# Kernel optimization log

Measured on AMD Instinct MI355X. Metric: run time of the kernel, lower is better.

## Reference

```python
import jax, jax.numpy as jnp
import numpy as np

N_NODES = 50000
N_EDGES = 600000
F_NODE = 128
F_EDGE = 32
MSG = 32


def setup_inputs() -> dict:
    key = jax.random.key(0)
    k1, k2, k3, k4, k5, k6, k7 = jax.random.split(key, 7)
    node_features = jax.random.normal(k1, (N_NODES, F_NODE), dtype=jnp.float32)
    edge_node_indices = jax.random.randint(k2, (2, N_EDGES), 0, N_NODES, dtype=jnp.int64)
    edge_features = jax.random.normal(k3, (N_EDGES, F_EDGE), dtype=jnp.float32)
    edge_in = 2 * F_NODE + F_EDGE  # 288
    node_in = F_NODE + MSG  # 160
    s_e = 1.0 / np.sqrt(edge_in)
    s_n = 1.0 / np.sqrt(node_in)
    We = jax.random.uniform(k4, (edge_in, MSG), dtype=jnp.float32, minval=-s_e, maxval=s_e)
    be = jax.random.uniform(k5, (MSG,), dtype=jnp.float32, minval=-s_e, maxval=s_e)
    Wn = jax.random.uniform(k6, (node_in, F_NODE), dtype=jnp.float32, minval=-s_n, maxval=s_n)
    bn = jax.random.uniform(k7, (F_NODE,), dtype=jnp.float32, minval=-s_n, maxval=s_n)
    return {
        "node_features": node_features,
        "edge_node_indices": edge_node_indices,
        "edge_features": edge_features,
        "We": We, "be": be, "Wn": Wn, "bn": bn,
    }


def reference(node_features, edge_node_indices, edge_features, We, be, Wn, bn):
    node0, node1 = edge_node_indices[0], edge_node_indices[1]
    # gather endpoint features per edge: [E, 2*Fn + Fe]
    msg_in = jnp.concatenate(
        [node_features[node0], node_features[node1], edge_features], axis=1
    )
    messages = jax.nn.relu(msg_in @ We + be)  # [E, MSG]
    # scatter-sum messages into source nodes (scatter index = node0)
    msg_sums = jax.ops.segment_sum(messages, node0, num_segments=node_features.shape[0])
    node_in = jnp.concatenate([node_features, msg_sums], axis=1)  # [N, Fn+MSG]
    return jax.nn.relu(node_in @ Wn + bn)  # [N, Fn]
```

## Files before the change

kernel.cpp:

```cpp
#include <hip/hip_runtime.h>

#define N_NODES 50000
#define N_EDGES 600000
#define F_NODE 128
#define F_EDGE 32
#define MSG 32
#define NPB 32
#define CHK 128
#define QB64 ((N_NODES + 63) / 64)
#define FBLOCKS ((N_NODES + NPB - 1) / NPB)
#define CBLOCKS ((N_EDGES + 255) / 256)

__device__ __forceinline__ unsigned short f2bf(float f) {
    union { float f; unsigned int u; } v; v.f = f;
    unsigned int r = v.u + 0x7fffu + ((v.u >> 16) & 1u);
    return (unsigned short)(r >> 16);
}

#define BAR_LGKM() do {                                           \
    asm volatile("s_waitcnt lgkmcnt(0)" ::: "memory");            \
    __builtin_amdgcn_s_barrier();                                 \
    asm volatile("" ::: "memory");                                \
} while (0)

__global__ __launch_bounds__(256)
void qcount_kernel(const float* __restrict__ nf,
                   const float* __restrict__ We,
                   const float* __restrict__ be,
                   const int* __restrict__ idx,
                   unsigned short* __restrict__ Q,
                   unsigned short* __restrict__ P0g,
                   int* __restrict__ deg)
{
    if (blockIdx.x >= QB64) {
        int e = (blockIdx.x - QB64) * 256 + threadIdx.x;
        if (e < N_EDGES) {
            int n = idx[e];
            if ((unsigned)n < (unsigned)N_NODES) atomicAdd(&deg[n], 1);
        }
        return;
    }
    __shared__ float sInT[32 * 64];
    __shared__ float sWeA[32 * 32];
    __shared__ float sWeB[32 * 32];

    const int tid = threadIdx.x;
    const int n0b = blockIdx.x * 64;
    const int ng = tid & 31;
    const int og = tid >> 5;

    float accA[2][4], accB[2][4];
#pragma unroll
    for (int i = 0; i < 2; ++i)
#pragma unroll
        for (int j = 0; j < 4; ++j) { accA[i][j] = 0.f; accB[i][j] = 0.f; }

    for (int kc = 0; kc < 4; ++kc) {
        __syncthreads();
        ((float4*)sWeA)[tid] = ((const float4*)(We + kc * 32 * MSG))[tid];
        ((float4*)sWeB)[tid] = ((const float4*)(We + (128 + kc * 32) * MSG))[tid];
        {
            int nl = tid >> 2, q = tid & 3;
            int n = n0b + nl; if (n >= N_NODES) n = N_NODES - 1;
            const float4* src4 = (const float4*)(nf + (size_t)n * F_NODE + kc * 32);
#pragma unroll
            for (int h = 0; h < 2; ++h) {
                float4 v = src4[q * 2 + h];
                int kl = q * 8 + h * 4;
                sInT[(kl + 0) * 64 + nl] = v.x;
                sInT[(kl + 1) * 64 + nl] = v.y;
                sInT[(kl + 2) * 64 + nl] = v.z;
                sInT[(kl + 3) * 64 + nl] = v.w;
            }
        }
        __syncthreads();
#pragma unroll
        for (int k = 0; k < 32; ++k) {
            float2 m = *(const float2*)&sInT[k * 64 + 2 * ng];
            float4 wa = *(const float4*)&sWeA[k * 32 + og * 4];
            float4 wb = *(const float4*)&sWeB[k * 32 + og * 4];
            accA[0][0] += m.x * wa.x; accA[0][1] += m.x * wa.y;
            accA[0][2] += m.x * wa.z; accA[0][3] += m.x * wa.w;
            accA[1][0] += m.y * wa.x; accA[1][1] += m.y * wa.y;
            accA[1][2] += m.y * wa.z; accA[1][3] += m.y * wa.w;
            accB[0][0] += m.x * wb.x; accB[0][1] += m.x * wb.y;
            accB[0][2] += m.x * wb.z; accB[0][3] += m.x * wb.w;
            accB[1][0] += m.y * wb.x; accB[1][1] += m.y * wb.y;
            accB[1][2] += m.y * wb.z; accB[1][3] += m.y * wb.w;
        }
    }
    float bloc[4];
#pragma unroll
    for (int j = 0; j < 4; ++j) bloc[j] = be[og * 4 + j];
#pragma unroll
    for (int i = 0; i < 2; ++i) {
        int n = n0b + 2 * ng + i;
        if (n < N_NODES) {
            ushort4 oq, op;
            oq.x = f2bf(accB[i][0]); oq.y = f2bf(accB[i][1]);
            oq.z = f2bf(accB[i][2]); oq.w = f2bf(accB[i][3]);
            op.x = f2bf(accA[i][0] + bloc[0]); op.y = f2bf(accA[i][1] + bloc[1]);
            op.z = f2bf(accA[i][2] + bloc[2]); op.w = f2bf(accA[i][3] + bloc[3]);
            *(ushort4*)(Q   + (size_t)n * MSG + og * 4) = oq;
            *(ushort4*)(P0g + (size_t)n * MSG + og * 4) = op;
        }
    }
}

__global__ __launch_bounds__(1024)
void scan_kernel(int* __restrict__ deg_cursor) {
    __shared__ int wsum[16];
    __shared__ int wpre[16];
    const int t = threadIdx.x;
    const int lane = t & 63;
    const int wid = t >> 6;
    const int N4 = N_NODES / 4;
    const int NT = (N4 + 1023) / 1024;
    int run = 0;
    int4 vnext = make_int4(0, 0, 0, 0);
    if (t < N4) vnext = ((const int4*)deg_cursor)[t];
    for (int tt = 0; tt < NT; ++tt) {
        int4 v = vnext;
        if (tt + 1 < NT) {
            int ni = (tt + 1) * 1024 + t;
            vnext = (ni < N4) ? ((const int4*)deg_cursor)[ni] : make_int4(0, 0, 0, 0);
        }
        int s = v.x + v.y + v.z + v.w;
        int x = s;
#pragma unroll
        for (int d = 1; d < 64; d <<= 1) {
            int u = __shfl_up(x, (unsigned)d, 64);
            if (lane >= d) x += u;
        }
        if (lane == 63) wsum[wid] = x;
        BAR_LGKM();
        if (wid == 0) {
            int ss = (lane < 16) ? wsum[lane] : 0;
#pragma unroll
            for (int d = 1; d < 16; d <<= 1) {
                int u = __shfl_up(ss, (unsigned)d, 64);
                if (lane >= d) ss += u;
            }
            if (lane < 16) wpre[lane] = ss;
        }
        BAR_LGKM();
        int wexcl = (wid > 0) ? wpre[wid - 1] : 0;
        int total = wpre[15];
        int i4 = tt * 1024 + t;
        if (i4 < N4) {
            int base = run + wexcl + (x - s);
            int4 o;
            o.x = base;
            o.y = base + v.x;
            o.z = base + v.x + v.y;
            o.w = base + v.x + v.y + v.z;
            ((int4*)deg_cursor)[i4] = o;
        }
        run += total;
        BAR_LGKM();
    }
}

__global__ void scatter_kernel(const int* __restrict__ idx, int* __restrict__ cursor,
                               int* __restrict__ perm) {
    int e = blockIdx.x * 256 + threadIdx.x;
    if (e < N_EDGES) {
        int n = idx[e];
        if ((unsigned)n >= (unsigned)N_NODES) n = 0;
        int p = atomicAdd(&cursor[n], 1);
        if ((unsigned)p < (unsigned)N_EDGES) perm[p] = e;
    }
}

__global__ __launch_bounds__(256, 5)
void fused_kernel(const float* __restrict__ nf,
                  const int* __restrict__ idx,
                  const float* __restrict__ ef,
                  const float* __restrict__ We,
                  const float* __restrict__ Wn,
                  const float* __restrict__ bn,
                  const int* __restrict__ perm,
                  const int* __restrict__ cursor,
                  const unsigned short* __restrict__ Q,
                  const unsigned short* __restrict__ P0g,
                  float* __restrict__ out)
{
    __shared__ __align__(16) float S[5284];
    float* sBuf = S;
    float* sWeC = S + 4096;
    float* sInT2 = S + 4096;
    int* sOff = (int*)(S + 5120);
    int* sNL  = (int*)(S + 5153);

    const int tid = threadIdx.x;
    const int n0b = blockIdx.x * NPB;

    if (tid <= NPB) {
        int nn = n0b + tid - 1;
        int v;
        if (nn < 0) v = 0;
        else { if (nn >= N_NODES) nn = N_NODES - 1; v = cursor[nn]; }
        if (v < 0) v = 0;
        if (v > N_EDGES) v = N_EDGES;
        sOff[tid] = v;
    }
    ((float4*)sWeC)[tid] = ((const float4*)(We + 256 * MSG))[tid];
    __syncthreads();

    const int rs = sOff[0];
    const int re = sOff[NPB];

    float msum[4];
#pragma unroll
    for (int j = 0; j < 4; ++j) msum[j] = 0.f;
    const int rnl = tid >> 3;
    const int rq4 = (tid & 7) * 4;
    const int gx  = (rq4 >> 3) << 2;

    const int eg = tid & 63;
    const int og = tid >> 6;
    const int el = tid >> 1;
    const int h2 = tid & 1;

    int n1r = 0;
    int pe_next = 0, pe_next2 = 0;
    float4 efr[4];
#pragma unroll
    for (int q = 0; q < 4; ++q) efr[q] = make_float4(0.f, 0.f, 0.f, 0.f);

    if (rs < re) {
        int e0 = rs + el;
        int pe0 = 0;
        if (e0 < re) {
            pe0 = perm[e0];
            if ((unsigned)pe0 >= (unsigned)N_EDGES) pe0 = 0;
            if (h2 == 0) {
                int tn = idx[N_EDGES + pe0];
                if ((unsigned)tn >= (unsigned)N_NODES) tn = 0;
                n1r = tn;
            }
        }
        const float4* ef4 = (const float4*)(ef + (size_t)pe0 * F_EDGE + h2 * 16);
#pragma unroll
        for (int q = 0; q < 4; ++q) efr[q] = ef4[q];
        int e1 = rs + CHK + el;
        if (e1 < re) {
            int p = perm[e1];
            if ((unsigned)p >= (unsigned)N_EDGES) p = 0;
            pe_next = p;
        }
        pe_next2 = pe_next;
    }

    for (int cs = rs; cs < re; cs += CHK) {
        BAR_LGKM();
        pe_next = pe_next2;
        {
#pragma unroll
            for (int q = 0; q < 4; ++q) {
                float4 v = efr[q];
                int g = (h2 * 2 + (q >> 1)) & 3;
                int ctw = ((el & ~3) ^ (g << 2)) + (el & 3);
                int r0 = (h2 * 16 + q * 4) * CHK;
                sBuf[r0 + 0 * CHK + ctw] = v.x;
                sBuf[r0 + 1 * CHK + ctw] = v.y;
                sBuf[r0 + 2 * CHK + ctw] = v.z;
                sBuf[r0 + 3 * CHK + ctw] = v.w;
            }
            if (h2 == 0) {
                int e = cs + el;
                int ln = 0;
                if (e < re) {
                    int lo = 0, hi = NPB;
#pragma unroll
                    for (int s = 0; s < 5; ++s) {
                        int mid = (lo + hi) >> 1;
                        if (sOff[mid] <= e) lo = mid; else hi = mid;
                    }
                    ln = lo;
                }
                sNL[el] = (ln << 20) | n1r;
            }
            int e1 = cs + CHK + el;
            if (e1 < re) {
                int pe1 = pe_next;
                if (h2 == 0) {
                    int tn = idx[N_EDGES + pe1];
                    if ((unsigned)tn >= (unsigned)N_NODES) tn = 0;
                    n1r = tn;
                }
                const float4* ef4 = (const float4*)(ef + (size_t)pe1 * F_EDGE + h2 * 16);
#pragma unroll
                for (int q = 0; q < 4; ++q) efr[q] = ef4[q];
            } else if (h2 == 0) n1r = 0;
            int e2 = cs + 2 * CHK + el;
            if (e2 < re) {
                int p = perm[e2];
                if ((unsigned)p >= (unsigned)N_EDGES) p = 0;
                pe_next2 = p;
            } else pe_next2 = 0;
        }
        BAR_LGKM();

        int nlv0 = sNL[2 * eg], nlv1 = sNL[2 * eg + 1];
        uint4 qv[2], pv[2];
        qv[0] = *(const uint4*)(Q   + (size_t)(nlv0 & 0xFFFFF) * MSG + og * 8);
        qv[1] = *(const uint4*)(Q   + (size_t)(nlv1 & 0xFFFFF) * MSG + og * 8);
        pv[0] = *(const uint4*)(P0g + (size_t)(n0b + (nlv0 >> 20)) * MSG + og * 8);
        pv[1] = *(const uint4*)(P0g + (size_t)(n0b + (nlv1 >> 20)) * MSG + og * 8);

        float acc[2][8];
#pragma unroll
        for (int i = 0; i < 2; ++i)
#pragma unroll
            for (int j = 0; j < 8; ++j) acc[i][j] = 0.f;

        const float* weB = sWeC + og * 8;
#pragma unroll
        for (int k = 0; k < 32; ++k) {
            int mb = k * CHK + (((2 * eg) & ~3) ^ (((k >> 3) & 3) << 2)) + ((2 * eg) & 3);
            float2 m = *(const float2*)&sBuf[mb];
            float4 w0 = *(const float4*)&weB[k * 32];
            float4 w1 = *(const float4*)&weB[k * 32 + 4];
            float ma[2] = { m.x, m.y };
            float wv[8] = { w0.x, w0.y, w0.z, w0.w, w1.x, w1.y, w1.z, w1.w };
#pragma unroll
            for (int i = 0; i < 2; ++i)
#pragma unroll
                for (int j = 0; j < 8; ++j) acc[i][j] += ma[i] * wv[j];
        }

        BAR_LGKM();

        {
            int sb = (((2 * eg) & ~3) ^ (og << 2)) + ((2 * eg) & 3);
#pragma unroll
            for (int j = 0; j < 8; ++j) {
                float sv[2];
#pragma unroll
                for (int i = 0; i < 2; ++i) {
                    unsigned qu = ((const unsigned*)&qv[i])[j >> 1];
                    unsigned pu = ((const unsigned*)&pv[i])[j >> 1];
                    float qf = __uint_as_float((j & 1) ? (qu & 0xffff0000u) : (qu << 16));
                    float pf = __uint_as_float((j & 1) ? (pu & 0xffff0000u) : (pu << 16));
                    sv[i] = fmaxf(acc[i][j] + pf + qf, 0.f);
                }
                float2 s2; s2.x = sv[0]; s2.y = sv[1];
                *(float2*)&sBuf[(og * 8 + j) * CHK + sb] = s2;
            }
        }
        BAR_LGKM();

        {
            int lo = sOff[rnl] - cs;     if (lo < 0) lo = 0;
            int hi = sOff[rnl + 1] - cs; if (hi > CHK) hi = CHK;
            for (int elr = lo; elr < hi; ++elr) {
                int ebase = ((elr & ~3) ^ gx) + (elr & 3);
#pragma unroll
                for (int j = 0; j < 4; ++j)
                    msum[j] += sBuf[(rq4 + j) * CHK + ebase];
            }
        }
    }

    const int ng2 = tid & 31;
    const int og2 = tid >> 5;

    float acc2[16];
#pragma unroll
    for (int j = 0; j < 16; ++j) acc2[j] = 0.f;

    for (int kc = 0; kc < 5; ++kc) {
        __syncthreads();
        {
            const float4* w4 = (const float4*)(Wn + (size_t)kc * 32 * 128);
            float4* s4 = (float4*)sBuf;
#pragma unroll
            for (int i = 0; i < 4; ++i) s4[tid + 256 * i] = w4[tid + 256 * i];
        }
        {
            if (kc < 4) {
                int nl = tid >> 3, q = tid & 7;
                int n = n0b + nl; if (n >= N_NODES) n = N_NODES - 1;
                float4 v = *(const float4*)(nf + (size_t)n * F_NODE + kc * 32 + q * 4);
#pragma unroll
                for (int h = 0; h < 4; ++h) {
                    int r = q * 4 + h;
                    sInT2[r * 32 + (nl ^ ((r & 7) << 2))] = (&v.x)[h];
                }
            } else {
#pragma unroll
                for (int h = 0; h < 4; ++h) {
                    int r = rq4 + h;
                    sInT2[r * 32 + (rnl ^ ((r & 7) << 2))] = msum[h];
                }
            }
        }
        __syncthreads();

#pragma unroll
        for (int k = 0; k < 32; ++k) {
            float m = sInT2[k * 32 + (ng2 ^ ((k & 7) << 2))];
            const float* wr = &sBuf[k * 128 + og2 * 16];
            float4 w0 = *(const float4*)&wr[0];
            float4 w1 = *(const float4*)&wr[4];
            float4 w2 = *(const float4*)&wr[8];
            float4 w3 = *(const float4*)&wr[12];
            float wv[16] = { w0.x,w0.y,w0.z,w0.w, w1.x,w1.y,w1.z,w1.w,
                             w2.x,w2.y,w2.z,w2.w, w3.x,w3.y,w3.z,w3.w };
#pragma unroll
            for (int j = 0; j < 16; ++j) acc2[j] += m * wv[j];
        }
    }

    {
        int n = n0b + ng2;
        if (n < N_NODES) {
            float* dst = out + (size_t)n * F_NODE + og2 * 16;
#pragma unroll
            for (int j = 0; j < 16; j += 4) {
                float4 v;
                v.x = fmaxf(acc2[j + 0] + bn[og2 * 16 + j + 0], 0.f);
                v.y = fmaxf(acc2[j + 1] + bn[og2 * 16 + j + 1], 0.f);
                v.z = fmaxf(acc2[j + 2] + bn[og2 * 16 + j + 2], 0.f);
                v.w = fmaxf(acc2[j + 3] + bn[og2 * 16 + j + 3], 0.f);
                *(float4*)(dst + j) = v;
            }
        }
    }
}

extern "C" void kernel_launch(void* const* d_in, const int* in_sizes, int n_in,
                              void* d_out, int out_size, void* d_ws, size_t ws_size,
                              hipStream_t stream) {
    const float* nf  = (const float*)d_in[0];
    const int*   idx = (const int*)d_in[1];
    const float* ef  = (const float*)d_in[2];
    const float* We  = (const float*)d_in[3];
    const float* be  = (const float*)d_in[4];
    const float* Wn  = (const float*)d_in[5];
    const float* bn  = (const float*)d_in[6];
    float* out = (float*)d_out;

    int* deg_cursor = (int*)d_ws;
    int* perm       = deg_cursor + N_NODES;
    unsigned short* Q   = (unsigned short*)(perm + N_EDGES);
    unsigned short* P0g = Q + (size_t)N_NODES * MSG;

    hipMemsetAsync(deg_cursor, 0, (size_t)N_NODES * sizeof(int), stream);

    qcount_kernel<<<QB64 + CBLOCKS, 256, 0, stream>>>(nf, We, be, idx, Q, P0g, deg_cursor);
    scan_kernel<<<1, 1024, 0, stream>>>(deg_cursor);
    scatter_kernel<<<CBLOCKS, 256, 0, stream>>>(idx, deg_cursor, perm);

    fused_kernel<<<FBLOCKS, 256, 0, stream>>>(
        nf, idx, ef, We, Wn, bn, perm, deg_cursor, Q, P0g, out);
}
```

Baseline: 298.2 us.

## Record atomic ranks in histogram, place edges without atomics, pack FMAs, stage P0 in LDS

The histogram pass now saves each edge's atomic return value as a rank, so the placement pass computes its slot as start plus rank and needs no second round of atomics. The scan output becomes an exclusive start array that fused_kernel reads directly. Accumulators in the edge and node GEMMs are rewritten as float2 vectors to encourage packed FMA instructions. The per-block P0 rows are staged once into shared memory instead of being gathered from global memory per edge chunk. The costs are an extra 600k-int rank array written and read, more shared memory per block, and lowering the launch-bounds occupancy hint from 5 to 4.

```diff
diff --git a/kernel.cpp b/kernel.cpp
--- a/kernel.cpp
+++ b/kernel.cpp
@@ -11,6 +11,8 @@
 #define FBLOCKS ((N_NODES + NPB - 1) / NPB)
 #define CBLOCKS ((N_EDGES + 255) / 256)
 
+typedef float v2f __attribute__((ext_vector_type(2)));
+
 __device__ __forceinline__ unsigned short f2bf(float f) {
     union { float f; unsigned int u; } v; v.f = f;
     unsigned int r = v.u + 0x7fffu + ((v.u >> 16) & 1u);
@@ -24,19 +26,21 @@
 } while (0)
 
 __global__ __launch_bounds__(256)
-void qcount_kernel(const float* __restrict__ nf,
-                   const float* __restrict__ We,
-                   const float* __restrict__ be,
-                   const int* __restrict__ idx,
-                   unsigned short* __restrict__ Q,
-                   unsigned short* __restrict__ P0g,
-                   int* __restrict__ deg)
+void hist_kernel(const float* __restrict__ nf,
+                 const float* __restrict__ We,
+                 const float* __restrict__ be,
+                 const int* __restrict__ idx,
+                 unsigned short* __restrict__ Q,
+                 unsigned short* __restrict__ P0g,
+                 int* __restrict__ deg,
+                 int* __restrict__ rank)
 {
     if (blockIdx.x >= QB64) {
         int e = (blockIdx.x - QB64) * 256 + threadIdx.x;
         if (e < N_EDGES) {
             int n = idx[e];
-            if ((unsigned)n < (unsigned)N_NODES) atomicAdd(&deg[n], 1);
+            if ((unsigned)n >= (unsigned)N_NODES) n = 0;
+            rank[e] = atomicAdd(&deg[n], 1);
         }
         return;
     }
@@ -49,11 +53,9 @@
     const int ng = tid & 31;
     const int og = tid >> 5;
 
-    float accA[2][4], accB[2][4];
-#pragma unroll
-    for (int i = 0; i < 2; ++i)
-#pragma unroll
-        for (int j = 0; j < 4; ++j) { accA[i][j] = 0.f; accB[i][j] = 0.f; }
+    v2f accA[4], accB[4];
+#pragma unroll
+    for (int j = 0; j < 4; ++j) { accA[j] = (v2f){0.f, 0.f}; accB[j] = (v2f){0.f, 0.f}; }
 
     for (int kc = 0; kc < 4; ++kc) {
         __syncthreads();
@@ -76,17 +78,13 @@
         __syncthreads();
 #pragma unroll
         for (int k = 0; k < 32; ++k) {
-            float2 m = *(const float2*)&sInT[k * 64 + 2 * ng];
+            v2f m = *(const v2f*)&sInT[k * 64 + 2 * ng];
             float4 wa = *(const float4*)&sWeA[k * 32 + og * 4];
             float4 wb = *(const float4*)&sWeB[k * 32 + og * 4];
-            accA[0][0] += m.x * wa.x; accA[0][1] += m.x * wa.y;
-            accA[0][2] += m.x * wa.z; accA[0][3] += m.x * wa.w;
-            accA[1][0] += m.y * wa.x; accA[1][1] += m.y * wa.y;
-            accA[1][2] += m.y * wa.z; accA[1][3] += m.y * wa.w;
-            accB[0][0] += m.x * wb.x; accB[0][1] += m.x * wb.y;
-            accB[0][2] += m.x * wb.z; accB[0][3] += m.x * wb.w;
-            accB[1][0] += m.y * wb.x; accB[1][1] += m.y * wb.y;
-            accB[1][2] += m.y * wb.z; accB[1][3] += m.y * wb.w;
+            accA[0] += m * wa.x; accA[1] += m * wa.y;
+            accA[2] += m * wa.z; accA[3] += m * wa.w;
+            accB[0] += m * wb.x; accB[1] += m * wb.y;
+            accB[2] += m * wb.z; accB[3] += m * wb.w;
         }
     }
     float bloc[4];
@@ -97,10 +95,10 @@
         int n = n0b + 2 * ng + i;
         if (n < N_NODES) {
             ushort4 oq, op;
-            oq.x = f2bf(accB[i][0]); oq.y = f2bf(accB[i][1]);
-            oq.z = f2bf(accB[i][2]); oq.w = f2bf(accB[i][3]);
-            op.x = f2bf(accA[i][0] + bloc[0]); op.y = f2bf(accA[i][1] + bloc[1]);
-            op.z = f2bf(accA[i][2] + bloc[2]); op.w = f2bf(accA[i][3] + bloc[3]);
+            oq.x = f2bf(accB[0][i]); oq.y = f2bf(accB[1][i]);
+            oq.z = f2bf(accB[2][i]); oq.w = f2bf(accB[3][i]);
+            op.x = f2bf(accA[0][i] + bloc[0]); op.y = f2bf(accA[1][i] + bloc[1]);
+            op.z = f2bf(accA[2][i] + bloc[2]); op.w = f2bf(accA[3][i] + bloc[3]);
             *(ushort4*)(Q   + (size_t)n * MSG + og * 4) = oq;
             *(ushort4*)(P0g + (size_t)n * MSG + og * 4) = op;
         }
@@ -161,18 +159,20 @@
     }
 }
 
-__global__ void scatter_kernel(const int* __restrict__ idx, int* __restrict__ cursor,
-                               int* __restrict__ perm) {
+__global__ void place_kernel(const int* __restrict__ idx,
+                             const int* __restrict__ startArr,
+                             const int* __restrict__ rank,
+                             int* __restrict__ perm) {
     int e = blockIdx.x * 256 + threadIdx.x;
     if (e < N_EDGES) {
         int n = idx[e];
         if ((unsigned)n >= (unsigned)N_NODES) n = 0;
-        int p = atomicAdd(&cursor[n], 1);
+        int p = startArr[n] + rank[e];
         if ((unsigned)p < (unsigned)N_EDGES) perm[p] = e;
     }
 }
 
-__global__ __launch_bounds__(256, 5)
+__global__ __launch_bounds__(256, 4)
 void fused_kernel(const float* __restrict__ nf,
                   const int* __restrict__ idx,
                   const float* __restrict__ ef,
@@ -180,31 +180,35 @@
                   const float* __restrict__ Wn,
                   const float* __restrict__ bn,
                   const int* __restrict__ perm,
-                  const int* __restrict__ cursor,
+                  const int* __restrict__ startArr,
                   const unsigned short* __restrict__ Q,
                   const unsigned short* __restrict__ P0g,
                   float* __restrict__ out)
 {
-    __shared__ __align__(16) float S[5284];
+    __shared__ __align__(16) float S[5796];
     float* sBuf = S;
     float* sWeC = S + 4096;
     float* sInT2 = S + 4096;
-    int* sOff = (int*)(S + 5120);
-    int* sNL  = (int*)(S + 5153);
+    unsigned short* sP0h = (unsigned short*)(S + 5120);
+    int* sOff = (int*)(S + 5632);
+    int* sNL  = (int*)(S + 5665);
 
     const int tid = threadIdx.x;
     const int n0b = blockIdx.x * NPB;
 
     if (tid <= NPB) {
-        int nn = n0b + tid - 1;
-        int v;
-        if (nn < 0) v = 0;
-        else { if (nn >= N_NODES) nn = N_NODES - 1; v = cursor[nn]; }
+        int nn = n0b + tid;
+        int v = (nn < N_NODES) ? startArr[nn] : N_EDGES;
         if (v < 0) v = 0;
         if (v > N_EDGES) v = N_EDGES;
         sOff[tid] = v;
     }
     ((float4*)sWeC)[tid] = ((const float4*)(We + 256 * MSG))[tid];
+    if (tid < 128) {
+        int r = tid >> 2, c = (tid & 3) * 8;
+        int n = n0b + r; if (n >= N_NODES) n = N_NODES - 1;
+        *(uint4*)(sP0h + r * MSG + c) = *(const uint4*)(P0g + (size_t)n * MSG + c);
+    }
     __syncthreads();
 
     const int rs = sOff[0];
@@ -303,36 +307,33 @@
         BAR_LGKM();
 
         int nlv0 = sNL[2 * eg], nlv1 = sNL[2 * eg + 1];
-        uint4 qv[2], pv[2];
-        qv[0] = *(const uint4*)(Q   + (size_t)(nlv0 & 0xFFFFF) * MSG + og * 8);
-        qv[1] = *(const uint4*)(Q   + (size_t)(nlv1 & 0xFFFFF) * MSG + og * 8);
-        pv[0] = *(const uint4*)(P0g + (size_t)(n0b + (nlv0 >> 20)) * MSG + og * 8);
-        pv[1] = *(const uint4*)(P0g + (size_t)(n0b + (nlv1 >> 20)) * MSG + og * 8);
-
-        float acc[2][8];
-#pragma unroll
-        for (int i = 0; i < 2; ++i)
-#pragma unroll
-            for (int j = 0; j < 8; ++j) acc[i][j] = 0.f;
+        uint4 qv[2];
+        qv[0] = *(const uint4*)(Q + (size_t)(nlv0 & 0xFFFFF) * MSG + og * 8);
+        qv[1] = *(const uint4*)(Q + (size_t)(nlv1 & 0xFFFFF) * MSG + og * 8);
+
+        v2f accv[8];
+#pragma unroll
+        for (int j = 0; j < 8; ++j) accv[j] = (v2f){0.f, 0.f};
 
         const float* weB = sWeC + og * 8;
 #pragma unroll
         for (int k = 0; k < 32; ++k) {
             int mb = k * CHK + (((2 * eg) & ~3) ^ (((k >> 3) & 3) << 2)) + ((2 * eg) & 3);
-            float2 m = *(const float2*)&sBuf[mb];
+            v2f m = *(const v2f*)&sBuf[mb];
             float4 w0 = *(const float4*)&weB[k * 32];
             float4 w1 = *(const float4*)&weB[k * 32 + 4];
-            float ma[2] = { m.x, m.y };
-            float wv[8] = { w0.x, w0.y, w0.z, w0.w, w1.x, w1.y, w1.z, w1.w };
-#pragma unroll
-            for (int i = 0; i < 2; ++i)
-#pragma unroll
-                for (int j = 0; j < 8; ++j) acc[i][j] += ma[i] * wv[j];
-        }
-
-        BAR_LGKM();
-
-        {
+            accv[0] += m * w0.x; accv[1] += m * w0.y;
+            accv[2] += m * w0.z; accv[3] += m * w0.w;
+            accv[4] += m * w1.x; accv[5] += m * w1.y;
+            accv[6] += m * w1.z; accv[7] += m * w1.w;
+        }
+
+        BAR_LGKM();
+
+        {
+            uint4 pv[2];
+            pv[0] = *(const uint4*)(sP0h + (nlv0 >> 20) * MSG + og * 8);
+            pv[1] = *(const uint4*)(sP0h + (nlv1 >> 20) * MSG + og * 8);
             int sb = (((2 * eg) & ~3) ^ (og << 2)) + ((2 * eg) & 3);
 #pragma unroll
             for (int j = 0; j < 8; ++j) {
@@ -343,7 +344,7 @@
                     unsigned pu = ((const unsigned*)&pv[i])[j >> 1];
                     float qf = __uint_as_float((j & 1) ? (qu & 0xffff0000u) : (qu << 16));
                     float pf = __uint_as_float((j & 1) ? (pu & 0xffff0000u) : (pu << 16));
-                    sv[i] = fmaxf(acc[i][j] + pf + qf, 0.f);
+                    sv[i] = fmaxf(accv[j][i] + pf + qf, 0.f);
                 }
                 float2 s2; s2.x = sv[0]; s2.y = sv[1];
                 *(float2*)&sBuf[(og * 8 + j) * CHK + sb] = s2;
@@ -366,9 +367,9 @@
     const int ng2 = tid & 31;
     const int og2 = tid >> 5;
 
-    float acc2[16];
-#pragma unroll
-    for (int j = 0; j < 16; ++j) acc2[j] = 0.f;
+    v2f acc2v[8];
+#pragma unroll
+    for (int j = 0; j < 8; ++j) acc2v[j] = (v2f){0.f, 0.f};
 
     for (int kc = 0; kc < 5; ++kc) {
         __syncthreads();
@@ -406,10 +407,10 @@
             float4 w1 = *(const float4*)&wr[4];
             float4 w2 = *(const float4*)&wr[8];
             float4 w3 = *(const float4*)&wr[12];
-            float wv[16] = { w0.x,w0.y,w0.z,w0.w, w1.x,w1.y,w1.z,w1.w,
-                             w2.x,w2.y,w2.z,w2.w, w3.x,w3.y,w3.z,w3.w };
-#pragma unroll
-            for (int j = 0; j < 16; ++j) acc2[j] += m * wv[j];
+            v2f wp[8] = { {w0.x,w0.y},{w0.z,w0.w},{w1.x,w1.y},{w1.z,w1.w},
+                          {w2.x,w2.y},{w2.z,w2.w},{w3.x,w3.y},{w3.z,w3.w} };
+#pragma unroll
+            for (int h = 0; h < 8; ++h) acc2v[h] += wp[h] * m;
         }
     }
 
@@ -420,10 +421,10 @@
 #pragma unroll
             for (int j = 0; j < 16; j += 4) {
                 float4 v;
-                v.x = fmaxf(acc2[j + 0] + bn[og2 * 16 + j + 0], 0.f);
-                v.y = fmaxf(acc2[j + 1] + bn[og2 * 16 + j + 1], 0.f);
-                v.z = fmaxf(acc2[j + 2] + bn[og2 * 16 + j + 2], 0.f);
-                v.w = fmaxf(acc2[j + 3] + bn[og2 * 16 + j + 3], 0.f);
+                v.x = fmaxf(acc2v[(j + 0) >> 1][0] + bn[og2 * 16 + j + 0], 0.f);
+                v.y = fmaxf(acc2v[(j + 1) >> 1][1] + bn[og2 * 16 + j + 1], 0.f);
+                v.z = fmaxf(acc2v[(j + 2) >> 1][0] + bn[og2 * 16 + j + 2], 0.f);
+                v.w = fmaxf(acc2v[(j + 3) >> 1][1] + bn[og2 * 16 + j + 3], 0.f);
                 *(float4*)(dst + j) = v;
             }
         }
@@ -442,17 +443,18 @@
     const float* bn  = (const float*)d_in[6];
     float* out = (float*)d_out;
 
-    int* deg_cursor = (int*)d_ws;
-    int* perm       = deg_cursor + N_NODES;
+    int* deg  = (int*)d_ws;
+    int* rank = deg + N_NODES;
+    int* perm = rank + N_EDGES;
     unsigned short* Q   = (unsigned short*)(perm + N_EDGES);
     unsigned short* P0g = Q + (size_t)N_NODES * MSG;
 
-    hipMemsetAsync(deg_cursor, 0, (size_t)N_NODES * sizeof(int), stream);
-
-    qcount_kernel<<<QB64 + CBLOCKS, 256, 0, stream>>>(nf, We, be, idx, Q, P0g, deg_cursor);
-    scan_kernel<<<1, 1024, 0, stream>>>(deg_cursor);
-    scatter_kernel<<<CBLOCKS, 256, 0, stream>>>(idx, deg_cursor, perm);
+    hipMemsetAsync(deg, 0, (size_t)N_NODES * sizeof(int), stream);
+
+    hist_kernel<<<QB64 + CBLOCKS, 256, 0, stream>>>(nf, We, be, idx, Q, P0g, deg, rank);
+    scan_kernel<<<1, 1024, 0, stream>>>(deg);
+    place_kernel<<<CBLOCKS, 256, 0, stream>>>(idx, deg, rank, perm);
 
     fused_kernel<<<FBLOCKS, 256, 0, stream>>>(
-        nf, idx, ef, We, Wn, bn, perm, deg_cursor, Q, P0g, out);
-}
+        nf, idx, ef, We, Wn, bn, perm, deg, Q, P0g, out);
+}
```

After: 271.9 us. 1.1x faster.
